# Kernel tuning notes

Hardware: AMD Instinct MI355X
Metric: run time of the kernel (lower is better)

Reference implementation:

```python
import jax, jax.numpy as jnp
import numpy as np

M, NC, NT, DX = 8, 1024, 512, 3
CHUNK = 512          # chunk_size
N_STEPS = 8          # n_steps (tol=0.0 -> torch early-stop never fires)
LR = 0.1
B1, B2, EPS = 0.9, 0.999, 1e-8
SQRT5 = 5.0 ** 0.5
LOG2PI = float(np.log(2.0 * np.pi))
NOISE_LB = 1e-4      # gpytorch GreaterThan(1e-4) noise constraint


def setup_inputs():
    key = jax.random.key(0)
    k1, k2, k3 = jax.random.split(key, 3)
    return {
        "xc": jax.random.normal(k1, (M, NC, DX), jnp.float32),
        "yc": jax.random.normal(k2, (M, NC, 1), jnp.float32),
        "xt": jax.random.normal(k3, (M, NT, DX), jnp.float32),
    }


def _kernel(x1, x2, ls, outscale):
    # ScaleKernel(MaternKernel(nu=2.5)); ls: [m,1,1], outscale: [m]
    xs1, xs2 = x1 / ls, x2 / ls
    d2 = (jnp.sum(xs1 * xs1, -1)[:, :, None]
          + jnp.sum(xs2 * xs2, -1)[:, None, :]
          - 2.0 * jnp.einsum('mnd,mkd->mnk', xs1, xs2))
    d2 = jnp.clip(d2, 1e-12, None)   # clamp like gpytorch dist for grad safety
    d = jnp.sqrt(d2)
    k = (1.0 + SQRT5 * d + (5.0 / 3.0) * d2) * jnp.exp(-SQRT5 * d)
    return outscale[:, None, None] * k


def _constrained(params):
    ls = jax.nn.softplus(params["raw_ls"])                          # [m,1,1]
    outscale = jax.nn.softplus(params["raw_os"])                    # [m]
    noise = jax.nn.softplus(params["raw_noise"][:, 0]) + NOISE_LB   # [m]
    return ls, outscale, noise


def _nll(params, x, y):
    # sum over tasks of -ExactMarginalLogLikelihood (gpytorch divides by n)
    ls, outscale, noise = _constrained(params)
    n = x.shape[1]
    K = _kernel(x, x, ls, outscale) + noise[:, None, None] * jnp.eye(n, dtype=x.dtype)
    L = jnp.linalg.cholesky(K)
    diff = y - params["const"][:, None]
    alpha = jax.scipy.linalg.cho_solve((L, True), diff[..., None])[..., 0]
    quad = jnp.sum(diff * alpha, -1)
    logdet = 2.0 * jnp.sum(jnp.log(jnp.diagonal(L, axis1=-2, axis2=-1)), -1)
    mll = -0.5 * (quad + logdet + n * LOG2PI) / n
    return jnp.sum(-mll)


def _adam_step(carry, x_sub, y_sub):
    p, m_, v_, t = carry
    g = jax.grad(_nll)(p, x_sub, y_sub)
    t = t + 1.0
    tm = jax.tree_util.tree_map
    m_ = tm(lambda a, gg: B1 * a + (1.0 - B1) * gg, m_, g)
    v_ = tm(lambda a, gg: B2 * a + (1.0 - B2) * gg * gg, v_, g)
    bc1 = 1.0 - B1 ** t
    bc2 = 1.0 - B2 ** t
    p = tm(lambda pp, mm, vv: pp - LR * (mm / bc1) / (jnp.sqrt(vv / bc2) + EPS), p, m_, v_)
    return (p, m_, v_, t)


def _gp_forward(xc, yc, xt):
    y = yc[..., 0]                                    # [m, nc]
    zl = lambda s: jnp.zeros(s, jnp.float32)
    # gpytorch raw params initialize to 0
    params = {"raw_ls": zl((M, 1, 1)), "raw_os": zl((M,)),
              "raw_noise": zl((M, 1)), "const": zl((M,))}
    m_ = jax.tree_util.tree_map(jnp.zeros_like, params)
    v_ = jax.tree_util.tree_map(jnp.zeros_like, params)
    carry = (params, m_, v_, jnp.float32(0.0))
    for i in range(0, NC, CHUNK):                     # 'Expanding' strategy
        end = min(i + CHUNK, NC)
        x_sub, y_sub = xc[:, :end], y[:, :end]
        step = lambda c, _: (_adam_step(c, x_sub, y_sub), None)
        carry, _ = jax.lax.scan(step, carry, None, length=N_STEPS)
    params = carry[0]
    # posterior predictive with trained hypers (train data = full context)
    ls, outscale, noise = _constrained(params)
    Kcc = _kernel(xc, xc, ls, outscale) + noise[:, None, None] * jnp.eye(NC, dtype=xc.dtype)
    L = jnp.linalg.cholesky(Kcc)
    diff = y - params["const"][:, None]
    alpha = jax.scipy.linalg.cho_solve((L, True), diff[..., None])[..., 0]
    Ktc = _kernel(xt, xc, ls, outscale)               # [m, nt, nc]
    mean = params["const"][:, None] + jnp.einsum('mtn,mn->mt', Ktc, alpha)
    v = jax.scipy.linalg.solve_triangular(L, jnp.swapaxes(Ktc, 1, 2), lower=True)  # [m,nc,nt]
    var_f = outscale[:, None] - jnp.sum(v * v, axis=1)  # Matern(0)=1 -> prior diag = outputscale
    var = var_f + noise[:, None]                      # likelihood(f) adds observation noise
    return jnp.stack([mean, var])                     # [2, m, nt]


def reference(xc, yc, xt):
    return _gp_forward(xc, yc, xt)
```

## Files before the change

### kernel.cpp

```cpp
#include <hip/hip_runtime.h>
#include <math.h>

constexpr int MM = 8;
constexpr int NC = 1024;
constexpr int NT = 512;

constexpr size_t OFF_A     = (size_t)MM * 1024 * 1024;
constexpr size_t OFF_T     = OFF_A * 2;
constexpr size_t OFF_KTC   = OFF_T + (size_t)MM * 512 * 512;
constexpr size_t OFF_ALPHA = OFF_KTC + (size_t)MM * NT * NC;
constexpr size_t OFF_SCAL  = OFF_ALPHA + (size_t)MM * 1024;
constexpr size_t OFF_ACC   = OFF_SCAL + (size_t)MM * 32;

#define S5 2.2360679775f

__device__ __forceinline__ float sigmf(float x) { return 1.0f / (1.0f + expf(-x)); }
__device__ __forceinline__ float softplusf(float x) { return fmaxf(x, 0.0f) + log1pf(expf(-fabsf(x))); }

__device__ __forceinline__ void lt_decode(int x, int& i, int& j) {
  int ii = 0;
  while ((ii + 1) * (ii + 2) / 2 <= x) ++ii;
  i = ii; j = x - ii * (ii + 1) / 2;
}

struct SMem {
  float Ls[64 * 65];
  float Us[64 * 65];
  float Tt[32 * 33];
  float dvec[64];
  float As[16][68];
  float Bs[16][68];
  float xi[64][3];
  float xj[64][3];
  float ai[64];
  float aj[64];
  float red[4][4];
};

template <int TA, int TB>
__device__ __forceinline__ void gemm64(const float* __restrict__ A, int lda,
                                       const float* __restrict__ B, int ldb,
                                       int kBeg, int kEnd, float acc[4][4], SMem& sm) {
  int tid = threadIdx.x, tx = tid & 15, ty = tid >> 4;
  float ra[4], rb[4];
  auto ldAB = [&](int k0) {
#pragma unroll
    for (int q = 0; q < 4; ++q) {
      int e = tid + (q << 8);
      if (TA) { int kk = e >> 6, r = e & 63; ra[q] = A[(size_t)(k0 + kk) * lda + r]; }
      else    { int r = e >> 4, kk = e & 15; ra[q] = A[(size_t)r * lda + k0 + kk]; }
      if (TB) { int c = e >> 4, kk = e & 15; rb[q] = B[(size_t)c * ldb + k0 + kk]; }
      else    { int kk = e >> 6, c = e & 63; rb[q] = B[(size_t)(k0 + kk) * ldb + c]; }
    }
  };
  ldAB(kBeg);
  for (int k0 = kBeg; k0 < kEnd; k0 += 16) {
    __syncthreads();
#pragma unroll
    for (int q = 0; q < 4; ++q) {
      int e = tid + (q << 8);
      if (TA) sm.As[e >> 6][e & 63] = ra[q]; else sm.As[e & 15][e >> 4] = ra[q];
      if (TB) sm.Bs[e & 15][e >> 4] = rb[q]; else sm.Bs[e >> 6][e & 63] = rb[q];
    }
    __syncthreads();
    if (k0 + 16 < kEnd) ldAB(k0 + 16);
#pragma unroll
    for (int kk = 0; kk < 16; ++kk) {
      float a[4], b[4];
#pragma unroll
      for (int i = 0; i < 4; ++i) a[i] = sm.As[kk][ty * 4 + i];
#pragma unroll
      for (int j = 0; j < 4; ++j) b[j] = sm.Bs[kk][tx * 4 + j];
#pragma unroll
      for (int i = 0; i < 4; ++i)
#pragma unroll
        for (int j = 0; j < 4; ++j) acc[i][j] = fmaf(a[i], b[j], acc[i][j]);
    }
  }
}

__device__ void factor64(SMem& sm, float* Uout, int ldu) {
  int tid = threadIdx.x;
  int tx = tid & 15, ty = tid >> 4;
  for (int j = 0; j < 63; ++j) {
    float rinv = 1.0f / sm.Ls[j * 65 + j];
    for (int i = j + 1 + ty; i < 64; i += 16) {
      float lij = sm.Ls[i * 65 + j] * rinv;
      for (int c = j + 1 + tx; c <= i; c += 16) sm.Ls[i * 65 + c] -= lij * sm.Ls[c * 65 + j];
    }
    __syncthreads();
  }
  if (tid < 64) sm.dvec[tid] = 1.0f / sqrtf(sm.Ls[tid * 65 + tid]);
  __syncthreads();
  for (int e = tid; e < 4096; e += 256) { int r = e >> 6, c = e & 63; if (c <= r) sm.Ls[r * 65 + c] *= sm.dvec[c]; }
  __syncthreads();
  for (int e = tid; e < 64 * 65; e += 256) sm.Us[e] = 0.0f;
  __syncthreads();
  if (tid < 64) {
    int b = tid >> 5, c0 = tid & 31, base = b * 32, gc = base + c0;
    sm.Us[gc * 65 + gc] = 1.0f / sm.Ls[gc * 65 + gc];
    for (int r = c0 + 1; r < 32; ++r) {
      int gr = base + r;
      float acc = 0.0f;
      for (int l = c0; l < r; ++l) acc += sm.Ls[gr * 65 + base + l] * sm.Us[(base + l) * 65 + gc];
      sm.Us[gr * 65 + gc] = -acc / sm.Ls[gr * 65 + gr];
    }
  }
  __syncthreads();
  for (int e = tid; e < 1024; e += 256) {
    int r = e >> 5, c = e & 31;
    float acc = 0.0f;
    for (int l = c; l < 32; ++l) acc += sm.Ls[(32 + r) * 65 + l] * sm.Us[l * 65 + c];
    sm.Tt[r * 33 + c] = acc;
  }
  __syncthreads();
  for (int e = tid; e < 1024; e += 256) {
    int r = e >> 5, c = e & 31;
    float acc = 0.0f;
    for (int l = 0; l <= r; ++l) acc += sm.Us[(32 + r) * 65 + 32 + l] * sm.Tt[l * 33 + c];
    sm.Us[(32 + r) * 65 + c] = -acc;
  }
  __syncthreads();
  for (int e = tid; e < 4096; e += 256) { int r = e >> 6, c = e & 63; Uout[(size_t)r * ldu + c] = sm.Us[r * 65 + c]; }
}


__global__ __launch_bounds__(256) void k_init(float* ws) {
  int t = threadIdx.x;
  float* scal = ws + OFF_SCAL;
  float* acc = ws + OFF_ACC;
  if (t < MM) {
    float* s = scal + t * 32;
    for (int i = 0; i < 12; ++i) s[i] = 0.0f;
    float sp0 = 0.69314718056f;
    s[12] = sp0; s[13] = sp0; s[14] = sp0 + 1e-4f; s[15] = 0.0f;
  }
  if (t < MM * 8) acc[t] = 0.0f;
}

__global__ __launch_bounds__(256) void k_adam(const float* __restrict__ yc, float* ws,
                                              int pn, int tstep) {
  int m = blockIdx.x, tid = threadIdx.x;
  float* sT = ws + OFF_SCAL + m * 32;
  float* accp = ws + OFF_ACC + m * 8;
  const float* al = ws + OFF_ALPHA + (size_t)m * 1024;
  const float* ym = yc + (size_t)m * NC;
  __shared__ float red[4][4];
  float cm = sT[15];
  float t4 = 0, t5 = 0, t6 = 0;
  for (int i = tid; i < pn; i += 256) {
    float a = al[i];
    t4 = fmaf(a, a, t4); t5 += a; t6 = fmaf(ym[i] - cm, a, t6);
  }
  for (int off = 32; off; off >>= 1) {
    t4 += __shfl_down(t4, off); t5 += __shfl_down(t5, off); t6 += __shfl_down(t6, off);
  }
  int wid = tid >> 6, lane = tid & 63;
  if (lane == 0) { red[wid][0] = t4; red[wid][1] = t5; red[wid][2] = t6; }
  __syncthreads();
  if (tid == 0) {
    t4 = red[0][0] + red[1][0] + red[2][0] + red[3][0];
    t5 = red[0][1] + red[1][1] + red[2][1] + red[3][1];
    t6 = red[0][2] + red[1][2] + red[2][2] + red[3][2];
    float T1 = accp[0], T2 = accp[1], t3 = accp[2];
    float ls = sT[12], os = sT[13], noi = sT[14];
    float fn = (float)pn;
    float g_ls = 0.5f / fn * (T1 - T2);
    float g_os = 0.5f / (fn * os) * (fn - noi * t3 - t6 + noi * t4);
    float g_no = 0.5f / fn * (t3 - t4);
    float g_c = -t5 / fn;
    float gr[4];
    gr[0] = g_ls * sigmf(sT[0]);
    gr[1] = g_os * sigmf(sT[1]);
    gr[2] = g_no * sigmf(sT[2]);
    gr[3] = g_c;
    float bc1 = 1.0f - powf(0.9f, (float)tstep);
    float bc2 = 1.0f - powf(0.999f, (float)tstep);
#pragma unroll
    for (int i = 0; i < 4; ++i) {
      float mv = 0.9f * sT[4 + i] + 0.1f * gr[i];
      float vv = 0.999f * sT[8 + i] + 0.001f * gr[i] * gr[i];
      sT[4 + i] = mv; sT[8 + i] = vv;
      sT[i] = sT[i] - 0.1f * (mv / bc1) / (sqrtf(vv / bc2) + 1e-8f);
    }
    sT[12] = softplusf(sT[0]);
    sT[13] = softplusf(sT[1]);
    sT[14] = softplusf(sT[2]) + 1e-4f;
    sT[15] = sT[3];
  }
}

__global__ __launch_bounds__(256) void k_buildK(const float* __restrict__ xc, float* ws, int n) {
  __shared__ SMem sm;
  int job = blockIdx.x, m = blockIdx.y, tid = threadIdx.x;
  const float* xm = xc + (size_t)m * NC * 3;
  float* Km = ws + (size_t)m * 1048576;
  float* Am = ws + OFF_A + (size_t)m * 1048576;
  const float* sT = ws + OFF_SCAL + m * 32;
  float ls = sT[12], os = sT[13], noi = sT[14];
  float il2 = 1.0f / (ls * ls);
  if (job >= 1 && job <= 4) {
    int zi = (job - 1) * 256 + tid;
    if (zi < n) ws[OFF_ALPHA + (size_t)m * 1024 + zi] = 0.0f;
  }
  if (job == 5 && tid < 4) ws[OFF_ACC + m * 8 + tid] = 0.0f;
  int bi, bj; lt_decode(job, bi, bj);
  if (tid < 64) {
    int r = bi * 64 + tid;
    sm.xi[tid][0] = xm[r * 3 + 0]; sm.xi[tid][1] = xm[r * 3 + 1]; sm.xi[tid][2] = xm[r * 3 + 2];
  } else if (tid < 128) {
    int lr = tid - 64; int r = bj * 64 + lr;
    sm.xj[lr][0] = xm[r * 3 + 0]; sm.xj[lr][1] = xm[r * 3 + 1]; sm.xj[lr][2] = xm[r * 3 + 2];
  }
  __syncthreads();
  if (job == 0) {
    for (int e = tid; e < 4096; e += 256) {
      int r = e >> 6, c = e & 63;
      float d0 = sm.xi[r][0] - sm.xj[c][0], d1 = sm.xi[r][1] - sm.xj[c][1], d2 = sm.xi[r][2] - sm.xj[c][2];
      float r2 = d0 * d0 + d1 * d1 + d2 * d2;
      float z = fmaxf(r2 * il2, 1e-12f);
      float dd = sqrtf(z);
      float kv = os * (1.0f + S5 * dd + (5.0f / 3.0f) * z) * expf(-S5 * dd);
      if (r == c) kv += noi;
      sm.Ls[r * 65 + c] = kv;
    }
    __syncthreads();
    factor64(sm, Am, n);
  } else {
    for (int e = tid; e < 4096; e += 256) {
      int r = e >> 6, c = e & 63;
      float d0 = sm.xi[r][0] - sm.xj[c][0], d1 = sm.xi[r][1] - sm.xj[c][1], d2 = sm.xi[r][2] - sm.xj[c][2];
      float r2 = d0 * d0 + d1 * d1 + d2 * d2;
      float z = fmaxf(r2 * il2, 1e-12f);
      float dd = sqrtf(z);
      float kv = os * (1.0f + S5 * dd + (5.0f / 3.0f) * z) * expf(-S5 * dd);
      if (bi == bj && r == c) kv += noi;
      Km[(size_t)(bi * 64 + r) * n + bj * 64 + c] = kv;
    }
  }
}

__global__ __launch_bounds__(256) void k_trail(float* ws, int k, int n) {
  __shared__ SMem sm;
  int job = blockIdx.x, m = blockIdx.y, tid = threadIdx.x;
  int tx = tid & 15, ty = tid >> 4;
  float* Km = ws + (size_t)m * 1048576;
  float* Am = ws + OFF_A + (size_t)m * 1048576;
  const float* Linv = Am + (size_t)(k * 64) * n + k * 64;
  int di, dj; lt_decode(job, di, dj);
  int i = k + 1 + di, j = k + 1 + dj;
  float pp[4][4] = {};
  gemm64<0, 1>(Km + (size_t)(i * 64) * n + k * 64, n, Linv, n, 0, 64, pp, sm);
  __syncthreads();
#pragma unroll
  for (int ii = 0; ii < 4; ++ii)
#pragma unroll
    for (int jj = 0; jj < 4; ++jj) sm.Ls[(ty * 4 + ii) * 65 + tx * 4 + jj] = pp[ii][jj];
  if (di == dj) {
    float* P = Am + (size_t)(i * 64) * n + k * 64;
#pragma unroll
    for (int ii = 0; ii < 4; ++ii)
#pragma unroll
      for (int jj = 0; jj < 4; ++jj) P[(size_t)(ty * 4 + ii) * n + tx * 4 + jj] = pp[ii][jj];
  } else {
#pragma unroll
    for (int ii = 0; ii < 4; ++ii)
#pragma unroll
      for (int jj = 0; jj < 4; ++jj) pp[ii][jj] = 0.0f;
    gemm64<0, 1>(Km + (size_t)(j * 64) * n + k * 64, n, Linv, n, 0, 64, pp, sm);
#pragma unroll
    for (int ii = 0; ii < 4; ++ii)
#pragma unroll
      for (int jj = 0; jj < 4; ++jj) sm.Us[(ty * 4 + ii) * 65 + tx * 4 + jj] = pp[ii][jj];
  }
  __syncthreads();
  float acc[4][4] = {};
  {
    const float* Bsrc = (di == dj) ? sm.Ls : sm.Us;
    for (int l = 0; l < 64; ++l) {
      float a[4], b[4];
#pragma unroll
      for (int ii = 0; ii < 4; ++ii) a[ii] = sm.Ls[(ty * 4 + ii) * 65 + l];
#pragma unroll
      for (int jj = 0; jj < 4; ++jj) b[jj] = Bsrc[(tx * 4 + jj) * 65 + l];
#pragma unroll
      for (int ii = 0; ii < 4; ++ii)
#pragma unroll
        for (int jj = 0; jj < 4; ++jj) acc[ii][jj] = fmaf(a[ii], b[jj], acc[ii][jj]);
    }
  }
  float* C = Km + (size_t)(i * 64) * n + j * 64;
  if (job == 0) {
    __syncthreads();
#pragma unroll
    for (int ii = 0; ii < 4; ++ii)
#pragma unroll
      for (int jj = 0; jj < 4; ++jj)
        sm.Ls[(ty * 4 + ii) * 65 + tx * 4 + jj] =
            C[(size_t)(ty * 4 + ii) * n + tx * 4 + jj] - acc[ii][jj];
    __syncthreads();
    factor64(sm, Am + (size_t)((k + 1) * 64) * n + (k + 1) * 64, n);
  } else {
#pragma unroll
    for (int ii = 0; ii < 4; ++ii)
#pragma unroll
      for (int jj = 0; jj < 4; ++jj)
        C[(size_t)(ty * 4 + ii) * n + tx * 4 + jj] -= acc[ii][jj];
  }
}

__global__ __launch_bounds__(256) void k_trinv64(float* ws, int n) {
  __shared__ SMem sm;
  int p = blockIdx.x, m = blockIdx.y, tid = threadIdx.x;
  int tx = tid & 15, ty = tid >> 4;
  float* Am = ws + OFF_A + (size_t)m * 1048576;
  int rb = (2 * p + 1) * 64, cb = 2 * p * 64;
  for (int e = tid; e < 4096; e += 256) {
    int r = e >> 6, c = e & 63;
    sm.Ls[r * 65 + c] = Am[(size_t)(rb + r) * n + cb + c];
    sm.Us[r * 65 + c] = Am[(size_t)(cb + r) * n + cb + c];
  }
  __syncthreads();
  float tt[4][4] = {};
  for (int l = 0; l < 64; ++l) {
    float a[4], b[4];
#pragma unroll
    for (int ii = 0; ii < 4; ++ii) a[ii] = sm.Ls[(ty * 4 + ii) * 65 + l];
#pragma unroll
    for (int jj = 0; jj < 4; ++jj) b[jj] = sm.Us[l * 65 + tx * 4 + jj];
#pragma unroll
    for (int ii = 0; ii < 4; ++ii)
#pragma unroll
      for (int jj = 0; jj < 4; ++jj) tt[ii][jj] = fmaf(a[ii], b[jj], tt[ii][jj]);
  }
  __syncthreads();
#pragma unroll
  for (int ii = 0; ii < 4; ++ii)
#pragma unroll
    for (int jj = 0; jj < 4; ++jj) sm.Ls[(ty * 4 + ii) * 65 + tx * 4 + jj] = tt[ii][jj];
  for (int e = tid; e < 4096; e += 256) {
    int r = e >> 6, c = e & 63;
    sm.Us[r * 65 + c] = Am[(size_t)(rb + r) * n + rb + c];
  }
  __syncthreads();
  float oo[4][4] = {};
  for (int l = 0; l < 64; ++l) {
    float a[4], b[4];
#pragma unroll
    for (int ii = 0; ii < 4; ++ii) a[ii] = sm.Us[(ty * 4 + ii) * 65 + l];
#pragma unroll
    for (int jj = 0; jj < 4; ++jj) b[jj] = sm.Ls[l * 65 + tx * 4 + jj];
#pragma unroll
    for (int ii = 0; ii < 4; ++ii)
#pragma unroll
      for (int jj = 0; jj < 4; ++jj) oo[ii][jj] = fmaf(a[ii], b[jj], oo[ii][jj]);
  }
#pragma unroll
  for (int ii = 0; ii < 4; ++ii)
#pragma unroll
    for (int jj = 0; jj < 4; ++jj)
      Am[(size_t)(rb + ty * 4 + ii) * n + cb + tx * 4 + jj] = -oo[ii][jj];
}

__global__ __launch_bounds__(256) void k_trinvT(float* ws, int s, int n) {
  __shared__ SMem sm;
  int job = blockIdx.x, m = blockIdx.y;
  int tx = threadIdx.x & 15, ty = threadIdx.x >> 4;
  float* Am = ws + OFF_A + (size_t)m * 1048576;
  float* Tm = ws + OFF_T + (size_t)m * 262144;
  int st = s >> 6;
  int p = job / (st * st), rem = job % (st * st);
  int ti = rem / st, tj = rem % st;
  int base = p * 2 * s;
  float acc[4][4] = {};
  gemm64<0, 0>(Am + (size_t)(base + s + ti * 64) * n + base, n,
               Am + (size_t)base * n + base + tj * 64, n, tj * 64, s, acc, sm);
  float* C = Tm + (size_t)p * s * s + (size_t)(ti * 64) * s + tj * 64;
#pragma unroll
  for (int ii = 0; ii < 4; ++ii)
#pragma unroll
    for (int jj = 0; jj < 4; ++jj) C[(size_t)(ty * 4 + ii) * s + tx * 4 + jj] = acc[ii][jj];
}

__global__ __launch_bounds__(256) void k_trinvA(float* ws, int s, int n) {
  __shared__ SMem sm;
  int job = blockIdx.x, m = blockIdx.y;
  int tx = threadIdx.x & 15, ty = threadIdx.x >> 4;
  float* Am = ws + OFF_A + (size_t)m * 1048576;
  const float* Tm = ws + OFF_T + (size_t)m * 262144;
  int st = s >> 6;
  int p = job / (st * st), rem = job % (st * st);
  int ti = rem / st, tj = rem % st;
  int base = p * 2 * s;
  float acc[4][4] = {};
  gemm64<0, 0>(Am + (size_t)(base + s + ti * 64) * n + base + s, n,
               Tm + (size_t)p * s * s + tj * 64, s, 0, (ti + 1) * 64, acc, sm);
  float* C = Am + (size_t)(base + s + ti * 64) * n + base + tj * 64;
#pragma unroll
  for (int ii = 0; ii < 4; ++ii)
#pragma unroll
    for (int jj = 0; jj < 4; ++jj) C[(size_t)(ty * 4 + ii) * n + tx * 4 + jj] = -acc[ii][jj];
}

__global__ __launch_bounds__(256) void k_syrkAT(const float* __restrict__ yc, float* ws, int n) {
  __shared__ SMem sm;
  int job = blockIdx.x, m = blockIdx.y, tid = threadIdx.x;
  int tx = tid & 15, ty = tid >> 4;
  const float* Am = ws + OFF_A + (size_t)m * 1048576;
  float* Gm = ws + (size_t)m * 1048576;
  const float* ym = yc + (size_t)m * NC;
  float* accp = ws + OFF_ACC + m * 8;
  float* al = ws + OFF_ALPHA + (size_t)m * 1024;
  float cm = ws[OFF_SCAL + m * 32 + 15];
  int ib, jb; lt_decode(job, ib, jb);
  if (tid < 64) sm.ai[tid] = ym[ib * 64 + tid] - cm;
  else if (tid < 128) sm.aj[tid - 64] = ym[jb * 64 + tid - 64] - cm;
  float acc[4][4] = {};
  gemm64<1, 0>(Am + ib * 64, n, Am + jb * 64, n, ib * 64, n, acc, sm);
#pragma unroll
  for (int ii = 0; ii < 4; ++ii)
#pragma unroll
    for (int jj = 0; jj < 4; ++jj) {
      int r = ty * 4 + ii, c = tx * 4 + jj;
      Gm[(size_t)(ib * 64 + r) * n + jb * 64 + c] = acc[ii][jj];
      if (ib != jb) Gm[(size_t)(jb * 64 + c) * n + ib * 64 + r] = acc[ii][jj];
    }
  if (ib == jb && tx == ty) {
    atomicAdd(&accp[2], acc[0][0] + acc[1][1] + acc[2][2] + acc[3][3]);
  }
  float rowp[4];
#pragma unroll
  for (int i = 0; i < 4; ++i) {
    float s = 0.0f;
#pragma unroll
    for (int j = 0; j < 4; ++j) s = fmaf(acc[i][j], sm.aj[tx * 4 + j], s);
    rowp[i] = s;
  }
  float colp[4];
  if (ib != jb) {
#pragma unroll
    for (int j = 0; j < 4; ++j) {
      float s = 0.0f;
#pragma unroll
      for (int i = 0; i < 4; ++i) s = fmaf(acc[i][j], sm.ai[ty * 4 + i], s);
      colp[j] = s;
    }
  }
  __syncthreads();
  float* redA = &sm.As[0][0];
  float* redB = &sm.Bs[0][0];
#pragma unroll
  for (int i = 0; i < 4; ++i) redA[(ty * 4 + i) * 16 + tx] = rowp[i];
  if (ib != jb) {
#pragma unroll
    for (int j = 0; j < 4; ++j) redB[(tx * 4 + j) * 16 + ty] = colp[j];
  }
  __syncthreads();
  if (tid < 64) {
    float s = 0.0f;
#pragma unroll
    for (int q = 0; q < 16; ++q) s += redA[tid * 16 + q];
    atomicAdd(&al[ib * 64 + tid], s);
    if (ib != jb) {
      float s2 = 0.0f;
#pragma unroll
      for (int q = 0; q < 16; ++q) s2 += redB[tid * 16 + q];
      atomicAdd(&al[jb * 64 + tid], s2);
    }
  }
}

__global__ __launch_bounds__(256) void k_reduce(const float* __restrict__ xc, float* ws, int n) {
  __shared__ SMem sm;
  int job = blockIdx.x, m = blockIdx.y, tid = threadIdx.x;
  const float* xm = xc + (size_t)m * NC * 3;
  const float* Gm = ws + (size_t)m * 1048576;
  const float* al = ws + OFF_ALPHA + (size_t)m * 1024;
  float* accp = ws + OFF_ACC + m * 8;
  const float* sT = ws + OFF_SCAL + m * 32;
  float ls = sT[12], os = sT[13];
  float il2 = 1.0f / (ls * ls);
  float c53 = (5.0f / 3.0f) * os / ls;
  int bi, bj; lt_decode(job, bi, bj);
  float w = (bi == bj) ? 1.0f : 2.0f;
  if (tid < 64) {
    int r = bi * 64 + tid;
    sm.xi[tid][0] = xm[r * 3 + 0]; sm.xi[tid][1] = xm[r * 3 + 1]; sm.xi[tid][2] = xm[r * 3 + 2];
    sm.ai[tid] = al[r];
  } else if (tid < 128) {
    int lr = tid - 64; int r = bj * 64 + lr;
    sm.xj[lr][0] = xm[r * 3 + 0]; sm.xj[lr][1] = xm[r * 3 + 1]; sm.xj[lr][2] = xm[r * 3 + 2];
    sm.aj[lr] = al[r];
  }
  __syncthreads();
  float a1 = 0.0f, a2 = 0.0f;
  for (int e = tid; e < 4096; e += 256) {
    int r = e >> 6, c = e & 63;
    float d0 = sm.xi[r][0] - sm.xj[c][0], d1 = sm.xi[r][1] - sm.xj[c][1], d2 = sm.xi[r][2] - sm.xj[c][2];
    float r2 = d0 * d0 + d1 * d1 + d2 * d2;
    float z = fmaxf(r2 * il2, 1e-12f);
    float dd = sqrtf(z);
    float Cv = c53 * z * (1.0f + S5 * dd) * expf(-S5 * dd);
    float g = Gm[(size_t)(bi * 64 + r) * n + bj * 64 + c];
    a1 = fmaf(g, Cv, a1);
    a2 = fmaf(sm.ai[r] * sm.aj[c], Cv, a2);
  }
  a1 *= w; a2 *= w;
  for (int off = 32; off; off >>= 1) { a1 += __shfl_down(a1, off); a2 += __shfl_down(a2, off); }
  int wid = tid >> 6, lane = tid & 63;
  if (lane == 0) { sm.red[wid][0] = a1; sm.red[wid][1] = a2; }
  __syncthreads();
  if (tid == 0) {
    a1 = sm.red[0][0] + sm.red[1][0] + sm.red[2][0] + sm.red[3][0];
    a2 = sm.red[0][1] + sm.red[1][1] + sm.red[2][1] + sm.red[3][1];
    atomicAdd(&accp[0], a1);
    atomicAdd(&accp[1], a2);
  }
}

__global__ __launch_bounds__(256) void k_buildKtc(const float* __restrict__ xt,
                                                  const float* __restrict__ xc, float* ws) {
  __shared__ SMem sm;
  int job = blockIdx.x, m = blockIdx.y, tid = threadIdx.x;
  const float* xtm = xt + (size_t)m * NT * 3;
  const float* xm = xc + (size_t)m * NC * 3;
  float* Kt = ws + OFF_KTC + (size_t)m * NT * NC;
  float* Tm = ws + OFF_T + (size_t)m * 262144;
  const float* sT = ws + OFF_SCAL + m * 32;
  float ls = sT[12], os = sT[13];
  float il2 = 1.0f / (ls * ls);
  if (job < 2) {
    int z = job * 256 + tid;
    Tm[z] = 0.0f; Tm[NT + z] = 0.0f;
  }
  int ti = job >> 4, tj = job & 15;
  if (tid < 64) {
    int r = ti * 64 + tid;
    sm.xi[tid][0] = xtm[r * 3 + 0]; sm.xi[tid][1] = xtm[r * 3 + 1]; sm.xi[tid][2] = xtm[r * 3 + 2];
  } else if (tid < 128) {
    int lr = tid - 64; int r = tj * 64 + lr;
    sm.xj[lr][0] = xm[r * 3 + 0]; sm.xj[lr][1] = xm[r * 3 + 1]; sm.xj[lr][2] = xm[r * 3 + 2];
  }
  __syncthreads();
  for (int e = tid; e < 4096; e += 256) {
    int r = e >> 6, c = e & 63;
    float d0 = sm.xi[r][0] - sm.xj[c][0], d1 = sm.xi[r][1] - sm.xj[c][1], d2 = sm.xi[r][2] - sm.xj[c][2];
    float r2 = d0 * d0 + d1 * d1 + d2 * d2;
    float z = fmaxf(r2 * il2, 1e-12f);
    float dd = sqrtf(z);
    float kv = os * (1.0f + S5 * dd + (5.0f / 3.0f) * z) * expf(-S5 * dd);
    Kt[(size_t)(ti * 64 + r) * NC + tj * 64 + c] = kv;
  }
}

__global__ __launch_bounds__(256) void k_predW(float* ws) {
  __shared__ SMem sm;
  int job = blockIdx.x, m = blockIdx.y, tid = threadIdx.x;
  int tx = tid & 15, ty = tid >> 4;
  const float* Kt = ws + OFF_KTC + (size_t)m * NT * NC;
  const float* Gm = ws + (size_t)m * 1048576;
  const float* al = ws + OFF_ALPHA + (size_t)m * 1024;
  float* S1 = ws + OFF_T + (size_t)m * 262144;
  float* S2 = S1 + NT;
  int ti = job >> 4, tj = job & 15;
  if (tid < 64) sm.aj[tid] = al[tj * 64 + tid];
  float acc[4][4] = {};
  gemm64<0, 0>(Kt + (size_t)(ti * 64) * NC, NC, Gm + tj * 64, 1024, 0, 1024, acc, sm);
  float s1p[4], s2p[4];
#pragma unroll
  for (int i = 0; i < 4; ++i) {
    float a1 = 0.0f, a2 = 0.0f;
    const float* kr = Kt + (size_t)(ti * 64 + ty * 4 + i) * NC + tj * 64;
#pragma unroll
    for (int j = 0; j < 4; ++j) {
      float kv = kr[tx * 4 + j];
      a1 = fmaf(kv, sm.aj[tx * 4 + j], a1);
      a2 = fmaf(kv, acc[i][j], a2);
    }
    s1p[i] = a1; s2p[i] = a2;
  }
  __syncthreads();
  float* redA = &sm.As[0][0];
  float* redB = &sm.Bs[0][0];
#pragma unroll
  for (int i = 0; i < 4; ++i) {
    redA[(ty * 4 + i) * 16 + tx] = s1p[i];
    redB[(ty * 4 + i) * 16 + tx] = s2p[i];
  }
  __syncthreads();
  if (tid < 64) {
    float a1 = 0.0f, a2 = 0.0f;
#pragma unroll
    for (int q = 0; q < 16; ++q) { a1 += redA[tid * 16 + q]; a2 += redB[tid * 16 + q]; }
    atomicAdd(&S1[ti * 64 + tid], a1);
    atomicAdd(&S2[ti * 64 + tid], a2);
  }
}

__global__ __launch_bounds__(256) void k_final(float* ws, float* out) {
  int m = blockIdx.y, t = blockIdx.x * 256 + threadIdx.x;
  const float* S1 = ws + OFF_T + (size_t)m * 262144;
  const float* S2 = S1 + NT;
  const float* sT = ws + OFF_SCAL + m * 32;
  if (t < NT) {
    out[(size_t)m * NT + t] = sT[15] + S1[t];
    out[(size_t)MM * NT + (size_t)m * NT + t] = sT[13] + sT[14] - S2[t];
  }
}

extern "C" void kernel_launch(void* const* d_in, const int* in_sizes, int n_in,
                              void* d_out, int out_size, void* d_ws, size_t ws_size,
                              hipStream_t stream) {
  const float* xc = (const float*)d_in[0];
  const float* yc = (const float*)d_in[1];
  const float* xt = (const float*)d_in[2];
  float* out = (float*)d_out;
  float* ws = (float*)d_ws;

  k_init<<<dim3(1), dim3(256), 0, stream>>>(ws);

  for (int step = 0; step < 17; ++step) {
    int n = step < 8 ? 512 : 1024;
    int nb = n >> 6;
    if (step > 0) {
      int pn = step <= 8 ? 512 : 1024;
      k_adam<<<dim3(MM), dim3(256), 0, stream>>>(yc, ws, pn, step);
    }
    k_buildK<<<dim3(nb * (nb + 1) / 2, MM), dim3(256), 0, stream>>>(xc, ws, n);
    for (int k = 0; k <= nb - 2; ++k) {
      int t = nb - 1 - k;
      k_trail<<<dim3(t * (t + 1) / 2, MM), dim3(256), 0, stream>>>(ws, k, n);
    }
    k_trinv64<<<dim3(n / 128, MM), dim3(256), 0, stream>>>(ws, n);
    for (int s = 128; s < n; s <<= 1) {
      int st = s >> 6, np = n / (2 * s);
      k_trinvT<<<dim3(np * st * st, MM), dim3(256), 0, stream>>>(ws, s, n);
      k_trinvA<<<dim3(np * st * st, MM), dim3(256), 0, stream>>>(ws, s, n);
    }
    k_syrkAT<<<dim3(nb * (nb + 1) / 2, MM), dim3(256), 0, stream>>>(yc, ws, n);
    if (step < 16) {
      k_reduce<<<dim3(nb * (nb + 1) / 2, MM), dim3(256), 0, stream>>>(xc, ws, n);
    }
  }

  k_buildKtc<<<dim3(128, MM), dim3(256), 0, stream>>>(xt, xc, ws);
  k_predW<<<dim3(128, MM), dim3(256), 0, stream>>>(ws);
  k_final<<<dim3(2, MM), dim3(256), 0, stream>>>(ws, out);

  (void)in_sizes; (void)n_in; (void)out_size; (void)ws_size;
}
```

Baseline: 19.74 ms.

## Fuse all GP training and prediction launches into one persistent kernel with grid barriers

Replaces the roughly five hundred separate kernel launches (Adam, K build, blocked Cholesky trail updates, triangular inverse stages, SYRK, reductions, prediction) with one persistent kernel of 512 blocks. Each former kernel becomes a device function whose jobs are spread over the blocks in a grid-stride loop, and phases are separated by a software grid barrier built on an atomic counter plus a generation word. The aim is to remove per-launch overhead and the idle gaps between the many small dependent launches. In exchange, every phase now pays a global barrier. Correctness depends on all 512 blocks being resident at once, which is not guaranteed without a cooperative launch, and launch_bounds(256,2) may add register pressure.

```diff
diff --git a/kernel.cpp b/kernel.cpp
--- a/kernel.cpp
+++ b/kernel.cpp
@@ -4,6 +4,7 @@
 constexpr int MM = 8;
 constexpr int NC = 1024;
 constexpr int NT = 512;
+constexpr int GRID = 512;
 
 constexpr size_t OFF_A     = (size_t)MM * 1024 * 1024;
 constexpr size_t OFF_T     = OFF_A * 2;
@@ -13,6 +14,28 @@
 constexpr size_t OFF_ACC   = OFF_SCAL + (size_t)MM * 32;
 
 #define S5 2.2360679775f
+
+__device__ unsigned g_cnt = 0;
+__device__ unsigned g_gen = 0;
+
+__device__ __forceinline__ void gbar() {
+  __syncthreads();
+  if (threadIdx.x == 0) {
+    __threadfence();
+    unsigned g = __hip_atomic_load(&g_gen, __ATOMIC_RELAXED, __HIP_MEMORY_SCOPE_AGENT);
+    unsigned a = __hip_atomic_fetch_add(&g_cnt, 1u, __ATOMIC_ACQ_REL, __HIP_MEMORY_SCOPE_AGENT);
+    if (a + 1u == (unsigned)GRID) {
+      __hip_atomic_store(&g_cnt, 0u, __ATOMIC_RELAXED, __HIP_MEMORY_SCOPE_AGENT);
+      __hip_atomic_store(&g_gen, g + 1u, __ATOMIC_RELEASE, __HIP_MEMORY_SCOPE_AGENT);
+    } else {
+      while (__hip_atomic_load(&g_gen, __ATOMIC_ACQUIRE, __HIP_MEMORY_SCOPE_AGENT) == g) {
+        __builtin_amdgcn_s_sleep(2);
+      }
+    }
+    __threadfence();
+  }
+  __syncthreads();
+}
 
 __device__ __forceinline__ float sigmf(float x) { return 1.0f / (1.0f + expf(-x)); }
 __device__ __forceinline__ float softplusf(float x) { return fmaxf(x, 0.0f) + log1pf(expf(-fabsf(x))); }
@@ -125,8 +148,7 @@
 }
 
 
-__global__ __launch_bounds__(256) void k_init(float* ws) {
-  int t = threadIdx.x;
+__device__ void d_init(float* ws, int t) {
   float* scal = ws + OFF_SCAL;
   float* acc = ws + OFF_ACC;
   if (t < MM) {
@@ -138,14 +160,13 @@
   if (t < MM * 8) acc[t] = 0.0f;
 }
 
-__global__ __launch_bounds__(256) void k_adam(const float* __restrict__ yc, float* ws,
-                                              int pn, int tstep) {
-  int m = blockIdx.x, tid = threadIdx.x;
+__device__ void d_adam(const float* __restrict__ yc, float* ws, int pn, int tstep,
+                       int m, int tid, SMem& sm) {
   float* sT = ws + OFF_SCAL + m * 32;
   float* accp = ws + OFF_ACC + m * 8;
   const float* al = ws + OFF_ALPHA + (size_t)m * 1024;
   const float* ym = yc + (size_t)m * NC;
-  __shared__ float red[4][4];
+  float (*red)[4] = sm.red;
   float cm = sT[15];
   float t4 = 0, t5 = 0, t6 = 0;
   for (int i = tid; i < pn; i += 256) {
@@ -190,9 +211,8 @@
   }
 }
 
-__global__ __launch_bounds__(256) void k_buildK(const float* __restrict__ xc, float* ws, int n) {
-  __shared__ SMem sm;
-  int job = blockIdx.x, m = blockIdx.y, tid = threadIdx.x;
+__device__ void d_buildK(const float* __restrict__ xc, float* ws, int n, int job, int m,
+                         int tid, SMem& sm) {
   const float* xm = xc + (size_t)m * NC * 3;
   float* Km = ws + (size_t)m * 1048576;
   float* Am = ws + OFF_A + (size_t)m * 1048576;
@@ -240,9 +260,7 @@
   }
 }
 
-__global__ __launch_bounds__(256) void k_trail(float* ws, int k, int n) {
-  __shared__ SMem sm;
-  int job = blockIdx.x, m = blockIdx.y, tid = threadIdx.x;
+__device__ void d_trail(float* ws, int k, int n, int job, int m, int tid, SMem& sm) {
   int tx = tid & 15, ty = tid >> 4;
   float* Km = ws + (size_t)m * 1048576;
   float* Am = ws + OFF_A + (size_t)m * 1048576;
@@ -309,9 +327,7 @@
   }
 }
 
-__global__ __launch_bounds__(256) void k_trinv64(float* ws, int n) {
-  __shared__ SMem sm;
-  int p = blockIdx.x, m = blockIdx.y, tid = threadIdx.x;
+__device__ void d_trinv64(float* ws, int n, int p, int m, int tid, SMem& sm) {
   int tx = tid & 15, ty = tid >> 4;
   float* Am = ws + OFF_A + (size_t)m * 1048576;
   int rb = (2 * p + 1) * 64, cb = 2 * p * 64;
@@ -362,10 +378,8 @@
       Am[(size_t)(rb + ty * 4 + ii) * n + cb + tx * 4 + jj] = -oo[ii][jj];
 }
 
-__global__ __launch_bounds__(256) void k_trinvT(float* ws, int s, int n) {
-  __shared__ SMem sm;
-  int job = blockIdx.x, m = blockIdx.y;
-  int tx = threadIdx.x & 15, ty = threadIdx.x >> 4;
+__device__ void d_trinvT(float* ws, int s, int n, int job, int m, int tid, SMem& sm) {
+  int tx = tid & 15, ty = tid >> 4;
   float* Am = ws + OFF_A + (size_t)m * 1048576;
   float* Tm = ws + OFF_T + (size_t)m * 262144;
   int st = s >> 6;
@@ -382,10 +396,8 @@
     for (int jj = 0; jj < 4; ++jj) C[(size_t)(ty * 4 + ii) * s + tx * 4 + jj] = acc[ii][jj];
 }
 
-__global__ __launch_bounds__(256) void k_trinvA(float* ws, int s, int n) {
-  __shared__ SMem sm;
-  int job = blockIdx.x, m = blockIdx.y;
-  int tx = threadIdx.x & 15, ty = threadIdx.x >> 4;
+__device__ void d_trinvA(float* ws, int s, int n, int job, int m, int tid, SMem& sm) {
+  int tx = tid & 15, ty = tid >> 4;
   float* Am = ws + OFF_A + (size_t)m * 1048576;
   const float* Tm = ws + OFF_T + (size_t)m * 262144;
   int st = s >> 6;
@@ -402,9 +414,8 @@
     for (int jj = 0; jj < 4; ++jj) C[(size_t)(ty * 4 + ii) * n + tx * 4 + jj] = -acc[ii][jj];
 }
 
-__global__ __launch_bounds__(256) void k_syrkAT(const float* __restrict__ yc, float* ws, int n) {
-  __shared__ SMem sm;
-  int job = blockIdx.x, m = blockIdx.y, tid = threadIdx.x;
+__device__ void d_syrkAT(const float* __restrict__ yc, float* ws, int n, int job, int m,
+                         int tid, SMem& sm) {
   int tx = tid & 15, ty = tid >> 4;
   const float* Am = ws + OFF_A + (size_t)m * 1048576;
   float* Gm = ws + (size_t)m * 1048576;
@@ -470,9 +481,8 @@
   }
 }
 
-__global__ __launch_bounds__(256) void k_reduce(const float* __restrict__ xc, float* ws, int n) {
-  __shared__ SMem sm;
-  int job = blockIdx.x, m = blockIdx.y, tid = threadIdx.x;
+__device__ void d_reduce(const float* __restrict__ xc, float* ws, int n, int job, int m,
+                         int tid, SMem& sm) {
   const float* xm = xc + (size_t)m * NC * 3;
   const float* Gm = ws + (size_t)m * 1048576;
   const float* al = ws + OFF_ALPHA + (size_t)m * 1024;
@@ -518,10 +528,8 @@
   }
 }
 
-__global__ __launch_bounds__(256) void k_buildKtc(const float* __restrict__ xt,
-                                                  const float* __restrict__ xc, float* ws) {
-  __shared__ SMem sm;
-  int job = blockIdx.x, m = blockIdx.y, tid = threadIdx.x;
+__device__ void d_buildKtc(const float* __restrict__ xt, const float* __restrict__ xc,
+                           float* ws, int job, int m, int tid, SMem& sm) {
   const float* xtm = xt + (size_t)m * NT * 3;
   const float* xm = xc + (size_t)m * NC * 3;
   float* Kt = ws + OFF_KTC + (size_t)m * NT * NC;
@@ -553,9 +561,7 @@
   }
 }
 
-__global__ __launch_bounds__(256) void k_predW(float* ws) {
-  __shared__ SMem sm;
-  int job = blockIdx.x, m = blockIdx.y, tid = threadIdx.x;
+__device__ void d_predW(float* ws, int job, int m, int tid, SMem& sm) {
   int tx = tid & 15, ty = tid >> 4;
   const float* Kt = ws + OFF_KTC + (size_t)m * NT * NC;
   const float* Gm = ws + (size_t)m * 1048576;
@@ -597,14 +603,112 @@
   }
 }
 
-__global__ __launch_bounds__(256) void k_final(float* ws, float* out) {
-  int m = blockIdx.y, t = blockIdx.x * 256 + threadIdx.x;
+__device__ __forceinline__ void d_final(const float* ws, float* out, int e) {
+  int m = e / NT, t = e % NT;
   const float* S1 = ws + OFF_T + (size_t)m * 262144;
   const float* S2 = S1 + NT;
   const float* sT = ws + OFF_SCAL + m * 32;
-  if (t < NT) {
-    out[(size_t)m * NT + t] = sT[15] + S1[t];
-    out[(size_t)MM * NT + (size_t)m * NT + t] = sT[13] + sT[14] - S2[t];
+  out[(size_t)m * NT + t] = sT[15] + S1[t];
+  out[(size_t)MM * NT + (size_t)m * NT + t] = sT[13] + sT[14] - S2[t];
+}
+
+__global__ __launch_bounds__(256, 2) void k_gp(const float* __restrict__ xc,
+                                               const float* __restrict__ yc,
+                                               const float* __restrict__ xt,
+                                               float* ws, float* out) {
+  __shared__ SMem sm;
+  const int bid = blockIdx.x;
+  const int G = gridDim.x;
+  const int tid = threadIdx.x;
+
+  if (bid == 0) d_init(ws, tid);
+  gbar();
+
+  for (int step = 0; step < 17; ++step) {
+    const int n = step < 8 ? 512 : 1024;
+    const int nb = n >> 6;
+
+    if (step > 0) {
+      if (bid < MM) d_adam(yc, ws, step <= 8 ? 512 : 1024, step, bid, tid, sm);
+      gbar();
+    }
+
+    {
+      const int tot = (nb * (nb + 1) / 2) * MM;
+      for (int q = bid; q < tot; q += G) {
+        __syncthreads();
+        d_buildK(xc, ws, n, q / MM, q % MM, tid, sm);
+      }
+      gbar();
+    }
+
+    for (int k = 0; k <= nb - 2; ++k) {
+      const int t = nb - 1 - k;
+      const int tot = (t * (t + 1) / 2) * MM;
+      for (int q = bid; q < tot; q += G) {
+        __syncthreads();
+        d_trail(ws, k, n, q / MM, q % MM, tid, sm);
+      }
+      gbar();
+    }
+
+    {
+      const int tot = (n / 128) * MM;
+      for (int q = bid; q < tot; q += G) {
+        __syncthreads();
+        d_trinv64(ws, n, q / MM, q % MM, tid, sm);
+      }
+      gbar();
+    }
+
+    for (int s = 128; s < n; s <<= 1) {
+      const int st = s >> 6;
+      const int np = n / (2 * s);
+      const int tot = np * st * st * MM;
+      for (int q = bid; q < tot; q += G) {
+        __syncthreads();
+        d_trinvT(ws, s, n, q / MM, q % MM, tid, sm);
+      }
+      gbar();
+      for (int q = bid; q < tot; q += G) {
+        __syncthreads();
+        d_trinvA(ws, s, n, q / MM, q % MM, tid, sm);
+      }
+      gbar();
+    }
+
+    {
+      const int tot = (nb * (nb + 1) / 2) * MM;
+      for (int q = bid; q < tot; q += G) {
+        __syncthreads();
+        d_syrkAT(yc, ws, n, q / MM, q % MM, tid, sm);
+      }
+      gbar();
+    }
+
+    if (step < 16) {
+      const int tot = (nb * (nb + 1) / 2) * MM;
+      for (int q = bid; q < tot; q += G) {
+        __syncthreads();
+        d_reduce(xc, ws, n, q / MM, q % MM, tid, sm);
+      }
+      gbar();
+    }
+  }
+
+  {
+    const int tot = 128 * MM;
+    for (int q = bid; q < tot; q += G) {
+      __syncthreads();
+      d_buildKtc(xt, xc, ws, q / MM, q % MM, tid, sm);
+    }
+    gbar();
+    for (int q = bid; q < tot; q += G) {
+      __syncthreads();
+      d_predW(ws, q / MM, q % MM, tid, sm);
+    }
+    gbar();
+    for (int e = bid * 256 + tid; e < MM * NT; e += G * 256) d_final(ws, out, e);
   }
 }
 
@@ -617,35 +721,7 @@
   float* out = (float*)d_out;
   float* ws = (float*)d_ws;
 
-  k_init<<<dim3(1), dim3(256), 0, stream>>>(ws);
-
-  for (int step = 0; step < 17; ++step) {
-    int n = step < 8 ? 512 : 1024;
-    int nb = n >> 6;
-    if (step > 0) {
-      int pn = step <= 8 ? 512 : 1024;
-      k_adam<<<dim3(MM), dim3(256), 0, stream>>>(yc, ws, pn, step);
-    }
-    k_buildK<<<dim3(nb * (nb + 1) / 2, MM), dim3(256), 0, stream>>>(xc, ws, n);
-    for (int k = 0; k <= nb - 2; ++k) {
-      int t = nb - 1 - k;
-      k_trail<<<dim3(t * (t + 1) / 2, MM), dim3(256), 0, stream>>>(ws, k, n);
-    }
-    k_trinv64<<<dim3(n / 128, MM), dim3(256), 0, stream>>>(ws, n);
-    for (int s = 128; s < n; s <<= 1) {
-      int st = s >> 6, np = n / (2 * s);
-      k_trinvT<<<dim3(np * st * st, MM), dim3(256), 0, stream>>>(ws, s, n);
-      k_trinvA<<<dim3(np * st * st, MM), dim3(256), 0, stream>>>(ws, s, n);
-    }
-    k_syrkAT<<<dim3(nb * (nb + 1) / 2, MM), dim3(256), 0, stream>>>(yc, ws, n);
-    if (step < 16) {
-      k_reduce<<<dim3(nb * (nb + 1) / 2, MM), dim3(256), 0, stream>>>(xc, ws, n);
-    }
-  }
-
-  k_buildKtc<<<dim3(128, MM), dim3(256), 0, stream>>>(xt, xc, ws);
-  k_predW<<<dim3(128, MM), dim3(256), 0, stream>>>(ws);
-  k_final<<<dim3(2, MM), dim3(256), 0, stream>>>(ws, out);
+  hipLaunchKernelGGL(k_gp, dim3(GRID), dim3(256), 0, stream, xc, yc, xt, ws, out);
 
   (void)in_sizes; (void)n_in; (void)out_size; (void)ws_size;
 }
```

Measured after the change: 57.22 ms. 190% more time.
